# Kernel optimization log

Measured on AMD Instinct MI355X. Metric: run time of the kernel, lower is better.

The kernel has to match this reference:

```python
import jax, jax.numpy as jnp
import numpy as np

B, N, D, H = 8, 1024, 768, 12
DH = D // H
SCALE = D ** (-0.5)  # standard_scale=False => dim**-0.5


def setup_inputs() -> dict:
    key = jax.random.key(0)
    ks = jax.random.split(key, 6)
    x = jax.random.normal(ks[0], (B, N, D), dtype=jnp.float32)
    gamma = jax.random.uniform(ks[1], (B,), dtype=jnp.float32)
    dist = jax.random.uniform(ks[2], (N, N), dtype=jnp.float32)
    W_qkv = jax.random.normal(ks[3], (D, 3 * D), dtype=jnp.float32) * (D ** -0.5)
    b_qkv = jnp.zeros((3 * D,), dtype=jnp.float32)
    W_proj = jax.random.normal(ks[4], (D, D), dtype=jnp.float32) * (D ** -0.5)
    b_proj = jnp.zeros((D,), dtype=jnp.float32)
    return {"x": x, "gamma": gamma, "dist": dist, "W_qkv": W_qkv,
            "b_qkv": b_qkv, "W_proj": W_proj, "b_proj": b_proj}


def reference(x, gamma, dist, W_qkv, b_qkv, W_proj, b_proj):
    # qkv projection: [B,N,3D] -> [3,B,H,N,DH]
    qkv = (x @ W_qkv + b_qkv).reshape(B, N, 3, H, DH).transpose(2, 0, 3, 1, 4)
    q, k, v = qkv[0], qkv[1], qkv[2]
    # scores [B,H,N,N] with learned per-batch distance bias
    scores = jnp.einsum('bhnd,bhmd->bhnm', q, k) * SCALE
    scores = scores - gamma[:, None, None, None] * dist[None, None, :, :]
    attn = jax.nn.softmax(scores, axis=-1)
    out = jnp.einsum('bhnm,bhmd->bhnd', attn, v)
    out = out.transpose(0, 2, 1, 3).reshape(B, N, D)  # [B,N,D]
    return out @ W_proj + b_proj
```

## Files before the change

### kernel.cpp

```cpp
#include <hip/hip_runtime.h>
#include <hip/hip_bf16.h>
#include <cstdint>
#include <cstddef>

#define B_  8
#define N_  1024
#define D_  768
#define H_  12
#define DH_ 64
#define M_  (B_*N_)
#define D3_ (3*D_)

typedef __bf16 bf16;
typedef __bf16 bf16x4 __attribute__((ext_vector_type(4)));
typedef __bf16 bf16x8 __attribute__((ext_vector_type(8)));
typedef float  floatx4 __attribute__((ext_vector_type(4)));
typedef float  floatx16 __attribute__((ext_vector_type(16)));
typedef unsigned int uint32x4 __attribute__((ext_vector_type(4)));

__device__ __forceinline__ void async16(const void* g, void* l) {
  __builtin_amdgcn_global_load_lds(
      (const __attribute__((address_space(1))) unsigned int*)g,
      (__attribute__((address_space(3))) unsigned int*)l, 16, 0, 0);
}

template <int Ncnt> __device__ __forceinline__ void wait_vmcnt() {
  asm volatile("s_waitcnt vmcnt(%0)" :: "n"(Ncnt) : "memory");
}

__global__ __launch_bounds__(256) void detect_small_k(
    const unsigned int* __restrict__ xraw, const void* bq, const void* bp,
    const void* gm, int* __restrict__ flag, bf16* bqd, bf16* bpd, float* gmd) {
  __shared__ int sc;
  if (threadIdx.x == 0) sc = 0;
  __syncthreads();
  int cnt = 0;
  for (int j = 0; j < 8; j++) {
    unsigned int w = xraw[threadIdx.x * 8 + j];
    unsigned int e = (w >> 7) & 0xFF;
    cnt += (e >= 100 && e <= 140) ? 1 : 0;
  }
  atomicAdd(&sc, cnt);
  __syncthreads();
  int f = (sc > 1024) ? 1 : 0;
  if (threadIdx.x == 0) *flag = f;
  for (int i = threadIdx.x; i < D3_; i += 256)
    bqd[i] = f ? ((const bf16*)bq)[i] : (bf16)((const float*)bq)[i];
  for (int i = threadIdx.x; i < D_; i += 256)
    bpd[i] = f ? ((const bf16*)bp)[i] : (bf16)((const float*)bp)[i];
  if (threadIdx.x < B_)
    gmd[threadIdx.x] = f ? (float)((const bf16*)gm)[threadIdx.x]
                         : ((const float*)gm)[threadIdx.x];
}

__device__ __forceinline__ void ingest_span(const void* src, bf16* dst, int f,
                                            long n4, long i0, long stride) {
  if (f) {
    const ushort2* s = (const ushort2*)src;
    ushort2* d = (ushort2*)dst;
    for (long i = i0; i < n4 * 2; i += stride) d[i] = s[i];
  } else {
    const float4* s = (const float4*)src;
    for (long i = i0; i < n4; i += stride) {
      float4 v = s[i];
      bf16x4 o = { (bf16)v.x, (bf16)v.y, (bf16)v.z, (bf16)v.w };
      *(bf16x4*)(dst + i * 4) = o;
    }
  }
}
#define XBLOCKS 1024
#define DBLOCKS 256
__global__ __launch_bounds__(256) void ingest2_k(const void* __restrict__ x,
                                                 bf16* __restrict__ xb,
                                                 const void* __restrict__ dist,
                                                 bf16* __restrict__ distb,
                                                 const int* __restrict__ flag) {
  int f = *flag;
  if (blockIdx.x < XBLOCKS) {
    long i0 = (long)blockIdx.x * 256 + threadIdx.x;
    ingest_span(x, xb, f, (long)M_ * D_ / 4, i0, (long)XBLOCKS * 256);
  } else {
    long i0 = (long)(blockIdx.x - XBLOCKS) * 256 + threadIdx.x;
    ingest_span(dist, distb, f, (long)N_ * N_ / 4, i0, (long)DBLOCKS * 256);
  }
}

__global__ __launch_bounds__(256) void ingest_wt_k(const void* srcA, bf16* dstA,
                                                   const void* srcB, bf16* dstB,
                                                   const int* __restrict__ flag,
                                                   int tilesA, int tcA) {
  __shared__ bf16 t[64][72];
  int f = *flag;
  int bid = blockIdx.x;
  const void* src; bf16* dst; int C;
  int tc;
  if (bid < tilesA) { src = srcA; dst = dstA; C = D3_; tc = tcA; }
  else { bid -= tilesA; src = srcB; dst = dstB; C = D_; tc = D_ / 64; }
  int c0 = (bid % tc) * 64, r0 = (bid / tc) * 64;
  int i = threadIdx.x >> 2, j0 = (threadIdx.x & 3) * 16;
  if (f) {
    const bf16* s = (const bf16*)src + (size_t)(r0 + i) * C + c0 + j0;
#pragma unroll
    for (int jj = 0; jj < 16; jj += 8) *(bf16x8*)&t[i][j0 + jj] = *(const bf16x8*)(s + jj);
  } else {
    const float4* s = (const float4*)((const float*)src + (size_t)(r0 + i) * C + c0 + j0);
#pragma unroll
    for (int jj = 0; jj < 4; jj++) {
      float4 v = s[jj];
      bf16x4 o = { (bf16)v.x, (bf16)v.y, (bf16)v.z, (bf16)v.w };
      *(bf16x4*)&t[i][j0 + jj * 4] = o;
    }
  }
  __syncthreads();
  bf16* d = dst + (size_t)(c0 + i) * D_ + r0 + j0;
#pragma unroll
  for (int jj = 0; jj < 16; jj++) d[jj] = t[j0 + jj][i];
}

template <int MODE, int TMI, int BYL>
__global__ __launch_bounds__(256) void gemm_bt(const bf16* __restrict__ A,
                                               const bf16* __restrict__ Bt,
                                               const bf16* __restrict__ bias,
                                               bf16* __restrict__ O0,
                                               bf16* __restrict__ O1,
                                               bf16* __restrict__ O2,
                                               float* __restrict__ OF,
                                               const int* __restrict__ flag,
                                               int Kdim) {
  constexpr int TM = TMI * 32;
  constexpr int NBUF = 4;
  constexpr int LPW = TMI / 2 + 2;
  constexpr int AELEM = NBUF * TM * 32;
  int id = blockIdx.x;
  int xcd = id & 7;
  int j = id >> 3;
  int bx = j / BYL;
  int by = xcd * BYL + (j % BYL);
  int n0 = bx * 128, m0 = by * TM;
  int tid = threadIdx.x, wave = tid >> 6, lane = tid & 63;
  int wm = (wave >> 1) * (TMI * 16), wn = (wave & 1) * 64;
  int cl = lane & 15, qd = lane >> 4;
  __shared__ __align__(16) bf16 sh[AELEM + NBUF * 128 * 32];
  floatx4 acc[TMI][4] = {};

  int srow = lane >> 2;
  int sko = ((lane & 3) ^ ((srow >> 1) & 3)) * 8;

  auto stage = [&](int tk, int buf) {
    int kt = tk * 32;
#pragma unroll
    for (int i = 0; i < TMI / 2; i++) {
      int c = wave * (TMI / 2) + i;
      int row = c * 16 + srow;
      async16(A + (size_t)(m0 + row) * Kdim + kt + sko,
              (char*)sh + buf * (TM * 64) + c * 1024);
    }
#pragma unroll
    for (int i = 0; i < 2; i++) {
      int c = wave * 2 + i;
      int row = c * 16 + srow;
      async16(Bt + (size_t)(n0 + row) * Kdim + kt + sko,
              (char*)sh + (size_t)AELEM * 2 + buf * 8192 + c * 1024);
    }
  };
  auto compute = [&](int buf) {
    const bf16* Ab = sh + buf * (TM * 32);
    const bf16* Bb = sh + AELEM + buf * (128 * 32);
    int ga = (cl >> 1) & 3;
    bf16x8 af[TMI], bfv[4];
#pragma unroll
    for (int mi = 0; mi < TMI; mi++)
      af[mi] = *(const bf16x8*)(Ab + (wm + mi * 16 + cl) * 32 + ((qd ^ ga) * 8));
#pragma unroll
    for (int ni = 0; ni < 4; ni++)
      bfv[ni] = *(const bf16x8*)(Bb + (wn + ni * 16 + cl) * 32 + ((qd ^ ga) * 8));
    __builtin_amdgcn_s_setprio(1);
#pragma unroll
    for (int mi = 0; mi < TMI; mi++)
#pragma unroll
      for (int ni = 0; ni < 4; ni++)
        acc[mi][ni] = __builtin_amdgcn_mfma_f32_16x16x32_bf16(af[mi], bfv[ni],
                                                              acc[mi][ni], 0, 0, 0);
    __builtin_amdgcn_s_setprio(0);
  };

  int NT = Kdim >> 5;
  stage(0, 0); stage(1, 1); stage(2, 2);
  for (int t = 0; t < NT - 3; ++t) {
    wait_vmcnt<2 * LPW>();
    __builtin_amdgcn_sched_barrier(0);
    __builtin_amdgcn_s_barrier();
    stage(t + 3, (t + 3) & 3);
    compute(t & 3);
  }
  wait_vmcnt<2 * LPW>();
  __builtin_amdgcn_sched_barrier(0);
  __builtin_amdgcn_s_barrier();
  compute((NT - 3) & 3);
  wait_vmcnt<LPW>();
  __builtin_amdgcn_sched_barrier(0);
  __builtin_amdgcn_s_barrier();
  compute((NT - 2) & 3);
  wait_vmcnt<0>();
  __builtin_amdgcn_sched_barrier(0);
  __builtin_amdgcn_s_barrier();
  compute((NT - 1) & 3);

  if constexpr (MODE == 0) {
    int t = n0 / D_;
    int h0 = (n0 % D_) >> 6;
    int b = m0 >> 10;
    int nbase = m0 & 1023;
    bf16* Ot = (t == 0) ? O0 : O1;
    float qs = (t == 0) ? (0.03608439182435161f * 1.4426950408889634f) : 1.f;
    __syncthreads();
#pragma unroll
    for (int hh = 0; hh < 2; hh++) {
      if ((wave >> 1) == hh) {
#pragma unroll
        for (int ni = 0; ni < 4; ni++) {
          int col = wn + ni * 16 + cl;
          float bv = (float)bias[n0 + col];
          int s = (col >> 3) & 7;
#pragma unroll
          for (int mi = 0; mi < TMI; mi++) {
            int qpos = (mi * 4 + qd) ^ s;
            bf16x4 w = { (bf16)((acc[mi][ni][0] + bv) * qs),
                         (bf16)((acc[mi][ni][1] + bv) * qs),
                         (bf16)((acc[mi][ni][2] + bv) * qs),
                         (bf16)((acc[mi][ni][3] + bv) * qs) };
            *(bf16x4*)((char*)sh + col * 144 + qpos * 8) = w;
          }
        }
      }
      __syncthreads();
      if (t < 2) {
#pragma unroll
        for (int it = 0; it < 4; it++) {
          int flat = it * 256 + tid;
          int rh = flat >> 3, jl = flat & 7;
          int hs = rh >> 6, rl = rh & 63;
          int cb = hs * 64 + jl * 8;
          int s = (cb >> 3) & 7;
          int q = rl >> 2, rr = rl & 3;
          bf16x8 w;
#pragma unroll
          for (int jj = 0; jj < 8; jj++)
            w[jj] = *(const bf16*)((char*)sh + (cb + jj) * 144 + ((q ^ s) * 8) + rr * 2);
          int ng = nbase + hh * 64 + rl;
          *(bf16x8*)(Ot + (((size_t)(b * H_ + h0 + hs) * N_ + ng) * DH_ + jl * 8)) = w;
        }
      } else {
#pragma unroll
        for (int it = 0; it < 4; it++) {
          int flat = it * 256 + tid;
          int col = flat >> 3, jl = flat & 7;
          int hs = col >> 6, d = col & 63;
          int s = (col >> 3) & 7;
          bf16x4 a0 = *(const bf16x4*)((char*)sh + col * 144 + (((2 * jl) ^ s) * 8));
          bf16x4 a1 = *(const bf16x4*)((char*)sh + col * 144 + (((2 * jl + 1) ^ s) * 8));
          bf16x8 w = { a0[0], a0[1], a0[2], a0[3], a1[0], a1[1], a1[2], a1[3] };
          int ng0 = nbase + hh * 64 + jl * 8;
          *(bf16x8*)(O2 + (((size_t)(b * H_ + h0 + hs) * DH_ + d) * N_ + ng0)) = w;
        }
      }
      __syncthreads();
    }
  } else {
    int fbf16 = *flag;
#pragma unroll
    for (int ni = 0; ni < 4; ni++) {
      int colb = n0 + wn + ni * 16;
      float bv = (float)bias[colb + cl];
#pragma unroll
      for (int mi = 0; mi < TMI; mi++) {
#pragma unroll
        for (int r = 0; r < 4; r++) {
          int row = m0 + wm + mi * 16 + qd * 4 + r;
          float v = acc[mi][ni][r] + bv;
          size_t oi = (size_t)row * D_ + colb + cl;
          if (fbf16) O0[oi] = (bf16)v;
          else       OF[oi] = v;
        }
      }
    }
  }
}

__global__ __launch_bounds__(256, 3) void attn_k(const bf16* __restrict__ Q,
                                                 const bf16* __restrict__ Kp,
                                                 const bf16* __restrict__ Vt,
                                                 const float* __restrict__ gammaf,
                                                 const bf16* __restrict__ dist,
                                                 bf16* __restrict__ O) {
  int bh = blockIdx.x % (B_ * H_);
  int q0 = (blockIdx.x / (B_ * H_)) * 128;
  int b = bh / H_, h = bh % H_;
  int tid = threadIdx.x, wave = tid >> 6, lane = tid & 63;
  int l5 = lane & 31, hh = lane >> 5, l7 = lane & 7;
  __shared__ __align__(16) bf16 Ks[128 * 64];
  __shared__ __align__(16) bf16 Vs[64 * 128];
  __shared__ float Ls[4 * 32];

  bf16x8 aq[4];
  {
    const bf16* Qg = Q + ((size_t)bh * N_ + q0 + wave * 32 + l5) * DH_ + hh * 8;
#pragma unroll
    for (int st = 0; st < 4; st++) aq[st] = *(const bf16x8*)(Qg + st * 16);
  }

  floatx16 oacc[2] = {};
  float lsum = 0.f;
  const float LOG2E = 1.4426950408889634f;
  float gl = gammaf[b] * LOG2E;

  const bf16* Kg0 = Kp + (size_t)bh * N_ * DH_;
  const bf16* Vg0 = Vt + (size_t)bh * DH_ * N_;
  const bf16* Dg  = dist + (size_t)(q0 + wave * 32 + l5) * N_ + hh * 4;

  int kofs[4], vofs[4];
  const bf16* kg[4]; const bf16* vg[4];
#pragma unroll
  for (int i = 0; i < 4; i++) {
    int id = tid + i * 256;
    int kr = id >> 3, ksl = id & 7;
    kofs[i] = kr * 128 + ((ksl ^ (kr & 7)) * 16);
    kg[i] = Kg0 + (size_t)kr * DH_ + ksl * 8;
    int vr = id >> 4, vsl = id & 15;
    vofs[i] = vr * 256 + ((vsl ^ (vr & 7)) * 16);
    vg[i] = Vg0 + (size_t)vr * N_ + vsl * 8;
  }
  int krd = l5 * 128;
  int vrd = l5 * 256;

  for (int t0 = 0; t0 < N_; t0 += 128) {
    bf16x8 kv[4], vv[4];
#pragma unroll
    for (int i = 0; i < 4; i++) kv[i] = *(const bf16x8*)(kg[i] + (size_t)t0 * DH_);
#pragma unroll
    for (int i = 0; i < 4; i++) vv[i] = *(const bf16x8*)(vg[i] + t0);
    bf16x4 ddr[16];
#pragma unroll
    for (int sub = 0; sub < 4; sub++)
#pragma unroll
      for (int jj = 0; jj < 4; jj++)
        ddr[sub * 4 + jj] = *(const bf16x4*)(Dg + t0 + sub * 32 + jj * 8);

    __syncthreads();
#pragma unroll
    for (int i = 0; i < 4; i++) *(bf16x8*)((char*)Ks + kofs[i]) = kv[i];
#pragma unroll
    for (int i = 0; i < 4; i++) *(bf16x8*)((char*)Vs + vofs[i]) = vv[i];
    __syncthreads();

#pragma unroll
    for (int sub = 0; sub < 4; sub++) {
      floatx16 s = {};
      __builtin_amdgcn_s_setprio(1);
#pragma unroll
      for (int st = 0; st < 4; st++) {
        bf16x8 ak = *(const bf16x8*)((char*)Ks + sub * 4096 + krd +
                                     (((st * 2 + hh) ^ l7) * 16));
        s = __builtin_amdgcn_mfma_f32_32x32x16_bf16(ak, aq[st], s, 0, 0, 0);
      }
      __builtin_amdgcn_s_setprio(0);

      float p[16];
#pragma unroll
      for (int r = 0; r < 16; r++) {
        float df = (float)ddr[sub * 4 + (r >> 2)][r & 3];
        p[r] = __builtin_exp2f(__builtin_fmaf(-gl, df, s[r]));
        lsum += p[r];
      }
      unsigned pw[8];
#pragma unroll
      for (int i = 0; i < 8; i++) {
        unsigned o_;
        asm("v_cvt_pk_bf16_f32 %0, %1, %2"
            : "=v"(o_) : "v"(p[2 * i]), "v"(p[2 * i + 1]));
        pw[i] = o_;
      }
      asm("v_permlane32_swap_b32 %0, %1" : "+v"(pw[0]), "+v"(pw[2]));
      asm("v_permlane32_swap_b32 %0, %1" : "+v"(pw[1]), "+v"(pw[3]));
      asm("v_permlane32_swap_b32 %0, %1" : "+v"(pw[4]), "+v"(pw[6]));
      asm("v_permlane32_swap_b32 %0, %1" : "+v"(pw[5]), "+v"(pw[7]));
      bf16x8 pa0, pa1;
      { uint32x4 u0 = { pw[0], pw[1], pw[2], pw[3] }; pa0 = *(bf16x8*)&u0; }
      { uint32x4 u1 = { pw[4], pw[5], pw[6], pw[7] }; pa1 = *(bf16x8*)&u1; }

      __builtin_amdgcn_s_setprio(1);
#pragma unroll
      for (int t = 0; t < 2; t++) {
        bf16x8 bv0 = *(const bf16x8*)((char*)Vs + t * 8192 + vrd +
                                      (((sub * 4 + hh) ^ l7) * 16));
        oacc[t] = __builtin_amdgcn_mfma_f32_32x32x16_bf16(pa0, bv0, oacc[t], 0, 0, 0);
        bf16x8 bv1 = *(const bf16x8*)((char*)Vs + t * 8192 + vrd +
                                      (((sub * 4 + 2 + hh) ^ l7) * 16));
        oacc[t] = __builtin_amdgcn_mfma_f32_32x32x16_bf16(pa1, bv1, oacc[t], 0, 0, 0);
      }
      __builtin_amdgcn_s_setprio(0);
    }
  }

  lsum += __shfl_xor(lsum, 32, 64);
  float inv = 1.f / lsum;
  Ls[wave * 32 + l5] = inv;
  __syncthreads();
  size_t obase = ((size_t)b * N_ + q0 + wave * 32) * D_ + h * DH_;
#pragma unroll
  for (int r = 0; r < 16; r++) {
    int qrow = (r & 3) + 8 * (r >> 2) + 4 * hh;
    float iv = Ls[wave * 32 + qrow];
#pragma unroll
    for (int t = 0; t < 2; t++)
      O[obase + (size_t)qrow * D_ + t * 32 + l5] = (bf16)(oacc[t][r] * iv);
  }
}

extern "C" void kernel_launch(void* const* d_in, const int* in_sizes, int n_in,
                              void* d_out, int out_size, void* d_ws, size_t ws_size,
                              hipStream_t stream) {
  const void* x     = d_in[0];
  const void* gamma = d_in[1];
  const void* dist  = d_in[2];
  const void* Wqkv  = d_in[3];
  const void* bqkv  = d_in[4];
  const void* Wproj = d_in[5];
  const void* bproj = d_in[6];

  char* ws = (char*)d_ws;
  size_t o = 0;
  int*   flag   = (int*)(ws + o);   o += 16;
  float* gammaf = (float*)(ws + o); o += 32;
  bf16*  xb     = (bf16*)(ws + o);  o += (size_t)M_ * D_ * 2;
  bf16*  distb  = (bf16*)(ws + o);  o += (size_t)N_ * N_ * 2;
  bf16*  bqkvb  = (bf16*)(ws + o);  o += (size_t)D3_ * 2;
  bf16*  bprojb = (bf16*)(ws + o);  o += (size_t)D_ * 2 + 8;
  bf16*  WqkvT  = (bf16*)(ws + o);  o += (size_t)D3_ * D_ * 2;
  bf16*  WprojT = (bf16*)(ws + o);  o += (size_t)D_ * D_ * 2;
  bf16*  Qp     = (bf16*)(ws + o);  o += (size_t)M_ * D_ * 2;
  bf16*  Kp     = (bf16*)(ws + o);  o += (size_t)M_ * D_ * 2;
  bf16*  Vtp    = (bf16*)(ws + o);  o += (size_t)M_ * D_ * 2;
  bf16*  Op     = (bf16*)(ws + o);  o += (size_t)M_ * D_ * 2;
  if (ws_size < o) return;

  detect_small_k<<<1, 256, 0, stream>>>((const unsigned int*)x, bqkv, bproj, gamma,
                                        flag, bqkvb, bprojb, gammaf);
  ingest2_k<<<XBLOCKS + DBLOCKS, 256, 0, stream>>>(x, xb, dist, distb, flag);
  int tilesA = (D3_ / 64) * (D_ / 64);
  int tilesB = (D_ / 64) * (D_ / 64);
  ingest_wt_k<<<tilesA + tilesB, 256, 0, stream>>>(Wqkv, WqkvT, Wproj, WprojT,
                                                   flag, tilesA, D3_ / 64);

  gemm_bt<0, 4, 8><<<18 * 64, 256, 0, stream>>>(
      xb, WqkvT, bqkvb, Qp, Kp, Vtp, nullptr, flag, D_);
  attn_k<<<dim3(B_ * H_ * (N_ / 128)), 256, 0, stream>>>(
      Qp, Kp, Vtp, gammaf, distb, Op);
  gemm_bt<1, 2, 16><<<6 * 128, 256, 0, stream>>>(
      Op, WprojT, bprojb, (bf16*)d_out, nullptr, nullptr, (float*)d_out, flag, D_);
}
```

Baseline: 249.5 us.

## Software-pipeline K/V and dist register prefetch across attention tiles

Restructures the attention main loop so the global loads of K, V and the distance-bias tile for the next 128-key block are issued right after the current block is written to LDS. The compute for the current block then overlaps those loads, hiding global-memory latency behind the MFMA and exp work. The loop is unrolled by two with ping-pong dist register buffers, which raises register pressure and could lower occupancy. It also issues one redundant wrapped-around prefetch on the last iteration.

After: 305.7 us. 22.6% more time.

```diff
diff --git a/kernel.cpp b/kernel.cpp
--- a/kernel.cpp
+++ b/kernel.cpp
@@ -333,74 +333,91 @@
   int krd = l5 * 128;
   int vrd = l5 * 256;
 
-  for (int t0 = 0; t0 < N_; t0 += 128) {
-    bf16x8 kv[4], vv[4];
-#pragma unroll
-    for (int i = 0; i < 4; i++) kv[i] = *(const bf16x8*)(kg[i] + (size_t)t0 * DH_);
-#pragma unroll
-    for (int i = 0; i < 4; i++) vv[i] = *(const bf16x8*)(vg[i] + t0);
-    bf16x4 ddr[16];
-#pragma unroll
-    for (int sub = 0; sub < 4; sub++)
-#pragma unroll
-      for (int jj = 0; jj < 4; jj++)
-        ddr[sub * 4 + jj] = *(const bf16x4*)(Dg + t0 + sub * 32 + jj * 8);
-
-    __syncthreads();
-#pragma unroll
-    for (int i = 0; i < 4; i++) *(bf16x8*)((char*)Ks + kofs[i]) = kv[i];
-#pragma unroll
-    for (int i = 0; i < 4; i++) *(bf16x8*)((char*)Vs + vofs[i]) = vv[i];
-    __syncthreads();
-
-#pragma unroll
-    for (int sub = 0; sub < 4; sub++) {
-      floatx16 s = {};
-      __builtin_amdgcn_s_setprio(1);
-#pragma unroll
-      for (int st = 0; st < 4; st++) {
-        bf16x8 ak = *(const bf16x8*)((char*)Ks + sub * 4096 + krd +
-                                     (((st * 2 + hh) ^ l7) * 16));
-        s = __builtin_amdgcn_mfma_f32_32x32x16_bf16(ak, aq[st], s, 0, 0, 0);
-      }
-      __builtin_amdgcn_s_setprio(0);
-
-      float p[16];
-#pragma unroll
-      for (int r = 0; r < 16; r++) {
-        float df = (float)ddr[sub * 4 + (r >> 2)][r & 3];
-        p[r] = __builtin_exp2f(__builtin_fmaf(-gl, df, s[r]));
-        lsum += p[r];
-      }
-      unsigned pw[8];
-#pragma unroll
-      for (int i = 0; i < 8; i++) {
-        unsigned o_;
-        asm("v_cvt_pk_bf16_f32 %0, %1, %2"
-            : "=v"(o_) : "v"(p[2 * i]), "v"(p[2 * i + 1]));
-        pw[i] = o_;
-      }
-      asm("v_permlane32_swap_b32 %0, %1" : "+v"(pw[0]), "+v"(pw[2]));
-      asm("v_permlane32_swap_b32 %0, %1" : "+v"(pw[1]), "+v"(pw[3]));
-      asm("v_permlane32_swap_b32 %0, %1" : "+v"(pw[4]), "+v"(pw[6]));
-      asm("v_permlane32_swap_b32 %0, %1" : "+v"(pw[5]), "+v"(pw[7]));
-      bf16x8 pa0, pa1;
-      { uint32x4 u0 = { pw[0], pw[1], pw[2], pw[3] }; pa0 = *(bf16x8*)&u0; }
-      { uint32x4 u1 = { pw[4], pw[5], pw[6], pw[7] }; pa1 = *(bf16x8*)&u1; }
-
-      __builtin_amdgcn_s_setprio(1);
-#pragma unroll
-      for (int t = 0; t < 2; t++) {
-        bf16x8 bv0 = *(const bf16x8*)((char*)Vs + t * 8192 + vrd +
-                                      (((sub * 4 + hh) ^ l7) * 16));
-        oacc[t] = __builtin_amdgcn_mfma_f32_32x32x16_bf16(pa0, bv0, oacc[t], 0, 0, 0);
-        bf16x8 bv1 = *(const bf16x8*)((char*)Vs + t * 8192 + vrd +
-                                      (((sub * 4 + 2 + hh) ^ l7) * 16));
-        oacc[t] = __builtin_amdgcn_mfma_f32_32x32x16_bf16(pa1, bv1, oacc[t], 0, 0, 0);
-      }
-      __builtin_amdgcn_s_setprio(0);
-    }
-  }
+  bf16x8 kv[4], vv[4];
+  bf16x4 ddrA[16], ddrB[16];
+#pragma unroll
+  for (int i = 0; i < 4; i++) kv[i] = *(const bf16x8*)(kg[i]);
+#pragma unroll
+  for (int i = 0; i < 4; i++) vv[i] = *(const bf16x8*)(vg[i]);
+#pragma unroll
+  for (int sub = 0; sub < 4; sub++)
+#pragma unroll
+    for (int jj = 0; jj < 4; jj++)
+      ddrA[sub * 4 + jj] = *(const bf16x4*)(Dg + sub * 32 + jj * 8);
+
+#define ATT_STEP(T0, DCUR, DNXT)                                              \
+  do {                                                                        \
+    __syncthreads();       \
+    _Pragma("unroll")                                                         \
+    for (int i = 0; i < 4; i++) *(bf16x8*)((char*)Ks + kofs[i]) = kv[i];      \
+    _Pragma("unroll")                                                         \
+    for (int i = 0; i < 4; i++) *(bf16x8*)((char*)Vs + vofs[i]) = vv[i];      \
+    __syncthreads();                                        \
+    int tn = (T0) + 128; tn = (tn < N_) ? tn : 0;   \
+    _Pragma("unroll")                                                         \
+    for (int i = 0; i < 4; i++)                                               \
+      kv[i] = *(const bf16x8*)(kg[i] + (size_t)tn * DH_);                     \
+    _Pragma("unroll")                                                         \
+    for (int i = 0; i < 4; i++) vv[i] = *(const bf16x8*)(vg[i] + tn);         \
+    _Pragma("unroll")                                                         \
+    for (int sub = 0; sub < 4; sub++)                                         \
+      _Pragma("unroll")                                                       \
+      for (int jj = 0; jj < 4; jj++)                                          \
+        DNXT[sub * 4 + jj] = *(const bf16x4*)(Dg + tn + sub * 32 + jj * 8);   \
+    _Pragma("unroll")                                                         \
+    for (int sub = 0; sub < 4; sub++) {                                       \
+      floatx16 s = {};                                                        \
+      __builtin_amdgcn_s_setprio(1);                                          \
+      _Pragma("unroll")                                                       \
+      for (int st = 0; st < 4; st++) {                                        \
+        bf16x8 ak = *(const bf16x8*)((char*)Ks + sub * 4096 + krd +           \
+                                     (((st * 2 + hh) ^ l7) * 16));            \
+        s = __builtin_amdgcn_mfma_f32_32x32x16_bf16(ak, aq[st], s, 0, 0, 0);  \
+      }                                                                       \
+      __builtin_amdgcn_s_setprio(0);                                          \
+      float p[16];                                                            \
+      _Pragma("unroll")                                                       \
+      for (int r = 0; r < 16; r++) {                                          \
+        float df = (float)DCUR[sub * 4 + (r >> 2)][r & 3];                    \
+        p[r] = __builtin_exp2f(__builtin_fmaf(-gl, df, s[r]));                \
+        lsum += p[r];                                                         \
+      }                                                                       \
+      unsigned pw[8];                                                         \
+      _Pragma("unroll")                                                       \
+      for (int i = 0; i < 8; i++) {                                           \
+        unsigned o_;                                                          \
+        asm("v_cvt_pk_bf16_f32 %0, %1, %2"                                    \
+            : "=v"(o_) : "v"(p[2 * i]), "v"(p[2 * i + 1]));                   \
+        pw[i] = o_;                                                           \
+      }                                                                       \
+      asm("v_permlane32_swap_b32 %0, %1" : "+v"(pw[0]), "+v"(pw[2]));         \
+      asm("v_permlane32_swap_b32 %0, %1" : "+v"(pw[1]), "+v"(pw[3]));         \
+      asm("v_permlane32_swap_b32 %0, %1" : "+v"(pw[4]), "+v"(pw[6]));         \
+      asm("v_permlane32_swap_b32 %0, %1" : "+v"(pw[5]), "+v"(pw[7]));         \
+      bf16x8 pa0, pa1;                                                        \
+      { uint32x4 u0 = { pw[0], pw[1], pw[2], pw[3] }; pa0 = *(bf16x8*)&u0; }  \
+      { uint32x4 u1 = { pw[4], pw[5], pw[6], pw[7] }; pa1 = *(bf16x8*)&u1; }  \
+      __builtin_amdgcn_s_setprio(1);                                          \
+      _Pragma("unroll")                                                       \
+      for (int t = 0; t < 2; t++) {                                           \
+        bf16x8 bv0 = *(const bf16x8*)((char*)Vs + t * 8192 + vrd +            \
+                                      (((sub * 4 + hh) ^ l7) * 16));          \
+        oacc[t] = __builtin_amdgcn_mfma_f32_32x32x16_bf16(pa0, bv0,           \
+                                                          oacc[t], 0, 0, 0);  \
+        bf16x8 bv1 = *(const bf16x8*)((char*)Vs + t * 8192 + vrd +            \
+                                      (((sub * 4 + 2 + hh) ^ l7) * 16));      \
+        oacc[t] = __builtin_amdgcn_mfma_f32_32x32x16_bf16(pa1, bv1,           \
+                                                          oacc[t], 0, 0, 0);  \
+      }                                                                       \
+      __builtin_amdgcn_s_setprio(0);                                          \
+    }                                                                         \
+  } while (0)
+
+  for (int t0 = 0; t0 < N_; t0 += 256) {
+    ATT_STEP(t0, ddrA, ddrB);
+    ATT_STEP(t0 + 128, ddrB, ddrA);
+  }
+#undef ATT_STEP
 
   lsum += __shfl_xor(lsum, 32, 64);
   float inv = 1.f / lsum;
```

## Load K fragments directly from global and double-buffer V in LDS

Applied to the files above, without the earlier changes.

Drops the K staging through shared memory. Each wave now loads its K MFMA operands straight from global into registers, ping-ponging between two register sets so the next sub-tile's K is prefetched during the current one. V moves to a double-buffered LDS array with its next tile prefetched into registers, which cuts the per-tile barriers from two to one. The dist bias loads are also spread out per sub-tile. In exchange, K is read redundantly from global or L2 by every wave with less coalesced access, and register pressure goes up under launch bounds of 3 blocks.

Result: slower. 278.2 us (+11.5%).

```diff
diff --git a/kernel.cpp b/kernel.cpp
--- a/kernel.cpp
+++ b/kernel.cpp
@@ -298,8 +298,7 @@
   int b = bh / H_, h = bh % H_;
   int tid = threadIdx.x, wave = tid >> 6, lane = tid & 63;
   int l5 = lane & 31, hh = lane >> 5, l7 = lane & 7;
-  __shared__ __align__(16) bf16 Ks[128 * 64];
-  __shared__ __align__(16) bf16 Vs[64 * 128];
+  __shared__ __align__(16) bf16 Vs[2][64 * 128];
   __shared__ float Ls[4 * 32];
 
   bf16x8 aq[4];
@@ -314,93 +313,99 @@
   const float LOG2E = 1.4426950408889634f;
   float gl = gammaf[b] * LOG2E;
 
-  const bf16* Kg0 = Kp + (size_t)bh * N_ * DH_;
   const bf16* Vg0 = Vt + (size_t)bh * DH_ * N_;
   const bf16* Dg  = dist + (size_t)(q0 + wave * 32 + l5) * N_ + hh * 4;
-
-  int kofs[4], vofs[4];
-  const bf16* kg[4]; const bf16* vg[4];
+  const bf16* Kf = Kp + (size_t)bh * N_ * DH_ + (size_t)l5 * DH_ + hh * 8;
+
+  int vofs[4];
+  const bf16* vg[4];
 #pragma unroll
   for (int i = 0; i < 4; i++) {
     int id = tid + i * 256;
-    int kr = id >> 3, ksl = id & 7;
-    kofs[i] = kr * 128 + ((ksl ^ (kr & 7)) * 16);
-    kg[i] = Kg0 + (size_t)kr * DH_ + ksl * 8;
     int vr = id >> 4, vsl = id & 15;
     vofs[i] = vr * 256 + ((vsl ^ (vr & 7)) * 16);
     vg[i] = Vg0 + (size_t)vr * N_ + vsl * 8;
   }
-  int krd = l5 * 128;
   int vrd = l5 * 256;
 
+  bf16x8 vv[4];
+#pragma unroll
+  for (int i = 0; i < 4; i++) vv[i] = *(const bf16x8*)(vg[i]);
+  bf16x8 akA[4], akB[4];
+#pragma unroll
+  for (int st = 0; st < 4; st++) akA[st] = *(const bf16x8*)(Kf + st * 16);
+
+#define SUB_BODY(SUB, AKC, AKN, T0C, NTK, NSB)                                \
+  do {                                                                        \
+    bf16x4 dd[4];   \
+    _Pragma("unroll")                                                         \
+    for (int jj = 0; jj < 4; jj++)                                            \
+      dd[jj] = *(const bf16x4*)(Dg + (T0C) + (SUB) * 32 + jj * 8);            \
+    _Pragma("unroll")  \
+    for (int st = 0; st < 4; st++)                                            \
+      AKN[st] = *(const bf16x8*)(Kf + (size_t)((NTK) + (NSB) * 32) * DH_ +    \
+                                 st * 16);                                    \
+    floatx16 s = {};                                                          \
+    __builtin_amdgcn_s_setprio(1);                                            \
+    _Pragma("unroll")                                                         \
+    for (int st = 0; st < 4; st++)                                            \
+      s = __builtin_amdgcn_mfma_f32_32x32x16_bf16(AKC[st], aq[st], s, 0, 0, 0);\
+    __builtin_amdgcn_s_setprio(0);                                            \
+    float p[16];                                                              \
+    _Pragma("unroll")                                                         \
+    for (int r = 0; r < 16; r++) {                                            \
+      float df = (float)dd[r >> 2][r & 3];                                    \
+      p[r] = __builtin_exp2f(__builtin_fmaf(-gl, df, s[r]));                  \
+      lsum += p[r];                                                           \
+    }                                                                         \
+    unsigned pw[8];                                                           \
+    _Pragma("unroll")                                                         \
+    for (int i = 0; i < 8; i++) {                                             \
+      unsigned o_;                                                            \
+      asm("v_cvt_pk_bf16_f32 %0, %1, %2"                                      \
+          : "=v"(o_) : "v"(p[2 * i]), "v"(p[2 * i + 1]));                     \
+      pw[i] = o_;                                                             \
+    }                                                                         \
+    asm("v_permlane32_swap_b32 %0, %1" : "+v"(pw[0]), "+v"(pw[2]));           \
+    asm("v_permlane32_swap_b32 %0, %1" : "+v"(pw[1]), "+v"(pw[3]));           \
+    asm("v_permlane32_swap_b32 %0, %1" : "+v"(pw[4]), "+v"(pw[6]));           \
+    asm("v_permlane32_swap_b32 %0, %1" : "+v"(pw[5]), "+v"(pw[7]));           \
+    bf16x8 pa0, pa1;         \
+    { uint32x4 u0 = { pw[0], pw[1], pw[2], pw[3] }; pa0 = *(bf16x8*)&u0; }    \
+    { uint32x4 u1 = { pw[4], pw[5], pw[6], pw[7] }; pa1 = *(bf16x8*)&u1; }    \
+    __builtin_amdgcn_s_setprio(1);                                            \
+    _Pragma("unroll")                                                         \
+    for (int t = 0; t < 2; t++) {                                             \
+      bf16x8 bv0 = *(const bf16x8*)((char*)Vs + cb + t * 8192 + vrd +         \
+                                    ((((SUB) * 4 + hh) ^ l7) * 16));          \
+      oacc[t] = __builtin_amdgcn_mfma_f32_32x32x16_bf16(pa0, bv0,             \
+                                                        oacc[t], 0, 0, 0);    \
+      bf16x8 bv1 = *(const bf16x8*)((char*)Vs + cb + t * 8192 + vrd +         \
+                                    ((((SUB) * 4 + 2 + hh) ^ l7) * 16));      \
+      oacc[t] = __builtin_amdgcn_mfma_f32_32x32x16_bf16(pa1, bv1,             \
+                                                        oacc[t], 0, 0, 0);    \
+    }                                                                         \
+    __builtin_amdgcn_s_setprio(0);                                            \
+  } while (0)
+
+  int cur = 0;
   for (int t0 = 0; t0 < N_; t0 += 128) {
-    bf16x8 kv[4], vv[4];
-#pragma unroll
-    for (int i = 0; i < 4; i++) kv[i] = *(const bf16x8*)(kg[i] + (size_t)t0 * DH_);
-#pragma unroll
-    for (int i = 0; i < 4; i++) vv[i] = *(const bf16x8*)(vg[i] + t0);
-    bf16x4 ddr[16];
-#pragma unroll
-    for (int sub = 0; sub < 4; sub++)
-#pragma unroll
-      for (int jj = 0; jj < 4; jj++)
-        ddr[sub * 4 + jj] = *(const bf16x4*)(Dg + t0 + sub * 32 + jj * 8);
-
+    int cb = cur * 16384;
+#pragma unroll
+    for (int i = 0; i < 4; i++)
+      *(bf16x8*)((char*)Vs + cb + vofs[i]) = vv[i];
     __syncthreads();
-#pragma unroll
-    for (int i = 0; i < 4; i++) *(bf16x8*)((char*)Ks + kofs[i]) = kv[i];
-#pragma unroll
-    for (int i = 0; i < 4; i++) *(bf16x8*)((char*)Vs + vofs[i]) = vv[i];
-    __syncthreads();
-
-#pragma unroll
-    for (int sub = 0; sub < 4; sub++) {
-      floatx16 s = {};
-      __builtin_amdgcn_s_setprio(1);
-#pragma unroll
-      for (int st = 0; st < 4; st++) {
-        bf16x8 ak = *(const bf16x8*)((char*)Ks + sub * 4096 + krd +
-                                     (((st * 2 + hh) ^ l7) * 16));
-        s = __builtin_amdgcn_mfma_f32_32x32x16_bf16(ak, aq[st], s, 0, 0, 0);
-      }
-      __builtin_amdgcn_s_setprio(0);
-
-      float p[16];
-#pragma unroll
-      for (int r = 0; r < 16; r++) {
-        float df = (float)ddr[sub * 4 + (r >> 2)][r & 3];
-        p[r] = __builtin_exp2f(__builtin_fmaf(-gl, df, s[r]));
-        lsum += p[r];
-      }
-      unsigned pw[8];
-#pragma unroll
-      for (int i = 0; i < 8; i++) {
-        unsigned o_;
-        asm("v_cvt_pk_bf16_f32 %0, %1, %2"
-            : "=v"(o_) : "v"(p[2 * i]), "v"(p[2 * i + 1]));
-        pw[i] = o_;
-      }
-      asm("v_permlane32_swap_b32 %0, %1" : "+v"(pw[0]), "+v"(pw[2]));
-      asm("v_permlane32_swap_b32 %0, %1" : "+v"(pw[1]), "+v"(pw[3]));
-      asm("v_permlane32_swap_b32 %0, %1" : "+v"(pw[4]), "+v"(pw[6]));
-      asm("v_permlane32_swap_b32 %0, %1" : "+v"(pw[5]), "+v"(pw[7]));
-      bf16x8 pa0, pa1;
-      { uint32x4 u0 = { pw[0], pw[1], pw[2], pw[3] }; pa0 = *(bf16x8*)&u0; }
-      { uint32x4 u1 = { pw[4], pw[5], pw[6], pw[7] }; pa1 = *(bf16x8*)&u1; }
-
-      __builtin_amdgcn_s_setprio(1);
-#pragma unroll
-      for (int t = 0; t < 2; t++) {
-        bf16x8 bv0 = *(const bf16x8*)((char*)Vs + t * 8192 + vrd +
-                                      (((sub * 4 + hh) ^ l7) * 16));
-        oacc[t] = __builtin_amdgcn_mfma_f32_32x32x16_bf16(pa0, bv0, oacc[t], 0, 0, 0);
-        bf16x8 bv1 = *(const bf16x8*)((char*)Vs + t * 8192 + vrd +
-                                      (((sub * 4 + 2 + hh) ^ l7) * 16));
-        oacc[t] = __builtin_amdgcn_mfma_f32_32x32x16_bf16(pa1, bv1, oacc[t], 0, 0, 0);
-      }
-      __builtin_amdgcn_s_setprio(0);
-    }
-  }
+    int tn = t0 + 128; tn = (tn < N_) ? tn : 0;
+#pragma unroll
+    for (int i = 0; i < 4; i++) vv[i] = *(const bf16x8*)(vg[i] + tn);
+
+    SUB_BODY(0, akA, akB, t0, t0, 1);
+    SUB_BODY(1, akB, akA, t0, t0, 2);
+    SUB_BODY(2, akA, akB, t0, t0, 3);
+    SUB_BODY(3, akB, akA, t0, tn, 0);
+    cur ^= 1;
+  }
+#undef SUB_BODY
 
   lsum += __shfl_xor(lsum, 32, 64);
   float inv = 1.f / lsum;
```
